# Optimization experiments

Measured on AMD Instinct MI355X. Metric: run time of the kernel, lower is better.

The kernel has to match this reference:

```python
import jax, jax.numpy as jnp
import numpy as np
from math import factorial

LMAX = 4
L2 = (LMAX + 1) ** 2                      # 25 spherical components
RES_B = 2 * (2 * LMAX + 1)                # 18 Gauss-Legendre beta nodes (exact for band 2*lmax products)
RES_A = 2 * (2 * LMAX + 1) + 1            # 19 uniform alpha nodes
EPS = 1e-5
# degree index of each (l,m) slot: [0,1,1,1,2,...]
L_IDX = np.repeat(np.arange(LMAX + 1), 2 * np.arange(LMAX + 1) + 1)


def _assoc_legendre(lmax, x):
    # Associated Legendre P_l^m(x) with Condon-Shortley phase; returns [l, m, B]
    B = x.shape[0]
    P = np.zeros((lmax + 1, lmax + 1, B))
    P[0, 0] = 1.0
    sx = np.sqrt(np.maximum(0.0, 1.0 - x * x))
    for m in range(1, lmax + 1):
        P[m, m] = -(2 * m - 1) * sx * P[m - 1, m - 1]
    for m in range(lmax):
        P[m + 1, m] = (2 * m + 1) * x * P[m, m]
    for m in range(lmax + 1):
        for l in range(m + 2, lmax + 1):
            P[l, m] = ((2 * l - 1) * x * P[l - 1, m] - (l + m - 1) * P[l - 2, m]) / (l - m)
    return P


def _build_sh(lmax, res_b, res_a):
    # Real orthonormal spherical harmonics sampled on a Gauss-Legendre x uniform-phi grid.
    ct, wb = np.polynomial.legendre.leggauss(res_b)       # cos(theta) nodes / weights
    phi = np.arange(res_a) * (2.0 * np.pi / res_a)
    P = _assoc_legendre(lmax, ct)
    l2 = (lmax + 1) ** 2
    Y = np.zeros((res_b, res_a, l2))
    for l in range(lmax + 1):
        for m in range(l + 1):
            Nlm = np.sqrt((2 * l + 1) / (4.0 * np.pi) * factorial(l - m) / factorial(l + m))
            if m == 0:
                Y[:, :, l * l + l] = (Nlm * P[l, 0])[:, None]
            else:
                base = np.sqrt(2.0) * Nlm * P[l, m]
                Y[:, :, l * l + l + m] = base[:, None] * np.cos(m * phi)[None, :]
                Y[:, :, l * l + l - m] = base[:, None] * np.sin(m * phi)[None, :]
    w = (wb[:, None] * np.full((1, res_a), 2.0 * np.pi / res_a)).reshape(-1)
    Yf = Y.reshape(-1, l2)
    return Yf, w

_Y_np, _w_np = _build_sh(LMAX, RES_B, RES_A)
TO_GRID = jnp.asarray(_Y_np, dtype=jnp.float32)                     # [G, L2]
FROM_GRID = jnp.asarray((_w_np[:, None] * _Y_np).T, dtype=jnp.float32)  # [L2, G], exact SH projection


def setup_inputs() -> dict:
    key = jax.random.key(0)
    ks = jax.random.split(key, 8)
    N, C = 6000, 128
    x = jax.random.normal(ks[0], (N, L2, C), dtype=jnp.float32)
    batch = jax.random.randint(ks[1], (N,), 0, 77)
    s = 1.0 / np.sqrt(C)
    return {
        "x": x,
        "batch": batch,
        "norm_w": jnp.ones((LMAX + 1, C), dtype=jnp.float32),
        "norm_b": jnp.zeros((C,), dtype=jnp.float32),
        "w1": jax.random.normal(ks[2], (LMAX + 1, C, C), dtype=jnp.float32) * s,
        "b1": jax.random.normal(ks[3], (C,), dtype=jnp.float32) * 0.02,
        "w_tp": jax.random.normal(ks[4], (LMAX + 1, C), dtype=jnp.float32),
        "w2": jax.random.normal(ks[5], (LMAX + 1, C, C), dtype=jnp.float32) * s,
        "b2": jax.random.normal(ks[6], (C,), dtype=jnp.float32) * 0.02,
    }


def _merge_layer_norm(x, w, b):
    # x: [N, L2, C]; center l=0 over channels, RMS over all components+channels, per-(l,C) affine.
    mean0 = jnp.mean(x[:, 0:1, :], axis=-1, keepdims=True)
    xc = jnp.concatenate([x[:, 0:1, :] - mean0, x[:, 1:, :]], axis=1)
    var = jnp.mean(xc * xc, axis=(1, 2), keepdims=True)
    xn = xc * jax.lax.rsqrt(var + EPS)
    out = xn * w[L_IDX][None]                      # [N, L2, C]
    return jnp.concatenate([out[:, 0:1, :] + b, out[:, 1:, :]], axis=1)


def _so3_linear(x, w, b):
    # per-degree linear: w [lmax+1, out, in]; bias on l=0 only
    W = w[L_IDX]                                    # [L2, out, in]
    y = jnp.einsum('nlc,lkc->nlk', x, W)
    return jnp.concatenate([y[:, 0:1, :] + b, y[:, 1:, :]], axis=1)


def _gaunt_self_tp(x, w_tp):
    # Gaunt self tensor-product (depthwise): pointwise square on the sphere,
    # exact projection back to SH (Gaunt-coefficient contraction), per-(l,C) weight.
    g = jnp.einsum('nlc,gl->ngc', x, TO_GRID)       # [N, G, C] to-grid
    y = jnp.einsum('ngc,lg->nlc', g * g, FROM_GRID)  # [N, L2, C] from-grid
    return y * w_tp[L_IDX][None]


def reference(x, batch, norm_w, norm_b, w1, b1, w_tp, w2, b2):
    x_res = x
    h = _merge_layer_norm(x, norm_w, norm_b)
    h = _so3_linear(h, w1, b1)
    h = _gaunt_self_tp(h, w_tp)
    h = _so3_linear(h, w2, b2)
    return h + x_res  # ffn_shortcut is Identity (num_in == num_out)
```

## Files before the change

kernel.cpp:

```cpp
#include <hip/hip_runtime.h>
#include <math.h>

#define L2C 25
#define CH  128
#define NB  8
#define GLB 7
#define GLA 13
#define NG  91
#define GPAD 96
#define KPAD 32
#define HROWS 242

typedef short bf16x8 __attribute__((ext_vector_type(8)));
typedef short short4v __attribute__((ext_vector_type(4)));
typedef int   i32x4  __attribute__((ext_vector_type(4)));
typedef float f32x4  __attribute__((ext_vector_type(4)));
typedef unsigned uint2v __attribute__((ext_vector_type(2)));

union frag_u { i32x4 i; bf16x8 h; };

__device__ inline short f2bf(float f) {
  union { float f; unsigned u; } v; v.f = f;
  unsigned r = (v.u + 0x7FFFu + ((v.u >> 16) & 1u)) >> 16;
  return (short)r;
}
__device__ inline float bf2f(short s) {
  union { unsigned u; float f; } v; v.u = ((unsigned)(unsigned short)s) << 16; return v.f;
}
__device__ inline unsigned cvt_pk_bf16(float lo, float hi) {
  unsigned r; asm("v_cvt_pk_bf16_f32 %0, %1, %2" : "=v"(r) : "v"(lo), "v"(hi)); return r;
}

__global__ void build_tables_kernel(short* __restrict__ toT, short* __restrict__ frT) {
  const int g = threadIdx.x;
  if (g >= GPAD) return;
  const double PI = 3.14159265358979323846;
  double Y[L2C];
  double wg = 0.0;
  if (g < NG) {
    const int b = g / GLA;
    const int a = g % GLA;
    double xx = cos(PI * (b + 0.75) / (GLB + 0.5));
    double pp = 1.0;
    for (int it = 0; it < 64; ++it) {
      double p0 = 1.0, p1 = xx;
      for (int j = 2; j <= GLB; ++j) { double p2 = ((2.0*j-1.0)*xx*p1 - (j-1.0)*p0)/j; p0 = p1; p1 = p2; }
      pp = GLB * (xx*p1 - p0) / (xx*xx - 1.0);
      xx -= p1 / pp;
    }
    { double p0 = 1.0, p1 = xx;
      for (int j = 2; j <= GLB; ++j) { double p2 = ((2.0*j-1.0)*xx*p1 - (j-1.0)*p0)/j; p0 = p1; p1 = p2; }
      pp = GLB * (xx*p1 - p0) / (xx*xx - 1.0); }
    const double wb = 2.0 / ((1.0 - xx*xx) * pp * pp);
    const double ct = xx;
    const double sx = sqrt(fmax(0.0, 1.0 - ct*ct));
    double P[5][5];
    P[0][0] = 1.0;
    for (int m = 1; m <= 4; ++m) P[m][m] = -(2.0*m - 1.0) * sx * P[m-1][m-1];
    for (int m = 0; m <= 3; ++m) P[m+1][m] = (2.0*m + 1.0) * ct * P[m][m];
    for (int m = 0; m <= 4; ++m)
      for (int l = m + 2; l <= 4; ++l)
        P[l][m] = ((2.0*l-1.0)*ct*P[l-1][m] - (l+m-1.0)*P[l-2][m]) / (l - m);
    const double fact[9] = {1,1,2,6,24,120,720,5040,40320};
    const double phi = (2.0*PI/GLA) * a;
    for (int l = 0; l <= 4; ++l)
      for (int m = 0; m <= l; ++m) {
        double Nlm = sqrt((2.0*l+1.0)/(4.0*PI) * fact[l-m]/fact[l+m]);
        if (m == 0) Y[l*l + l] = Nlm * P[l][0];
        else {
          double base = sqrt(2.0) * Nlm * P[l][m];
          Y[l*l + l + m] = base * cos((double)m * phi);
          Y[l*l + l - m] = base * sin((double)m * phi);
        }
      }
    wg = wb * (2.0*PI/GLA);
  }
  for (int l = 0; l < KPAD; ++l) {
    float tv = (g < NG && l < L2C) ? (float)Y[l] : 0.f;
    toT[g*KPAD + l] = f2bf(tv);
  }
  {
    const int hi = g >> 4, r = g & 15;
    const int ksv = hi >> 1, pa = hi & 1;
    const int lqv = r >> 2,  pb = r & 3;
    const int u  = pa*4 + pb;
    const int kg = ksv*32 + lqv*8 + u;
    for (int l = 0; l < KPAD; ++l)
      frT[l*GPAD + kg] = (g < NG && l < L2C) ? f2bf((float)(wg * Y[l])) : (short)0;
  }
}

__global__ void convert_w_kernel(const float* __restrict__ w1, const float* __restrict__ w2,
                                 short* __restrict__ wb1, short* __restrict__ wb2) {
  const int i = blockIdx.x * 256 + threadIdx.x;
  if (i < 5*CH*CH) { wb1[i] = f2bf(w1[i]); wb2[i] = f2bf(w2[i]); }
}

__global__ __launch_bounds__(512, 2) void eqv3_fused8(
    const float* __restrict__ x,
    const float* __restrict__ norm_w, const float* __restrict__ norm_b,
    const short* __restrict__ wb1, const float* __restrict__ b1,
    const float* __restrict__ w_tp,
    const short* __restrict__ wb2, const float* __restrict__ b2,
    const short* __restrict__ toT, const short* __restrict__ frT,
    float* __restrict__ out)
{
  __shared__ __align__(16) short hsh[16][HROWS][8];
  __shared__ __align__(16) short hg[NB][4][CH][8];

  const int tid  = threadIdx.x;
  const int w    = tid >> 6;
  const int lane = tid & 63;
  const int l16  = lane & 15;
  const int lq   = lane >> 4;
  const long n0  = (long)blockIdx.x * NB;
  const int k    = w*16 + l16;

  constexpr int LDEG[L2C] = {0,1,1,1,2,2,2,2,2,3,3,3,3,3,3,3,4,4,4,4,4,4,4,4,4};
  constexpr int BROW[5]   = {0,16,48,96,160};
  constexpr int NT[5]     = {1,2,3,4,5};

  {
    const i32x4 z = {0,0,0,0};
    #pragma unroll
    for (int n = 0; n < NB; ++n) *(i32x4*)&hg[n][3][k][0] = z;
  }

  {
    const float4* x4 = (const float4*)(x + (n0 + w)*(long)(L2C*CH));
    float4 xv[13];
    float s0 = 0.f, s0q = 0.f, sq = 0.f;
    #pragma unroll
    for (int it = 0; it < 13; ++it) {
      const int j = it*64 + lane;
      if (j < 800) {
        xv[it] = x4[j];
        const float t = xv[it].x*xv[it].x + xv[it].y*xv[it].y + xv[it].z*xv[it].z + xv[it].w*xv[it].w;
        if (j < 32) { s0 += xv[it].x + xv[it].y + xv[it].z + xv[it].w; s0q += t; }
        else        sq += t;
      }
    }
    #pragma unroll
    for (int o = 1; o < 64; o <<= 1) {
      s0  += __shfl_xor(s0,  o, 64);
      s0q += __shfl_xor(s0q, o, 64);
      sq  += __shfl_xor(sq,  o, 64);
    }
    const float mean0 = s0 * (1.f/CH);
    const float var   = (sq + s0q - CH*mean0*mean0) * (1.f/(L2C*CH));
    const float rstd  = rsqrtf(var + 1e-5f);
    #pragma unroll
    for (int it = 0; it < 13; ++it) {
      const int j = it*64 + lane;
      if (j < 800) {
        const int s = j >> 5;
        const int d = (int)sqrtf((float)s + 0.5f);
        const int row = 8*(s + d) + w;
        const int c32 = j & 31;
        const int c0  = c32 * 4;
        const float4 nw4 = ((const float4*)norm_w)[d*32 + c32];
        float a0 = xv[it].x, a1 = xv[it].y, a2 = xv[it].z, a3 = xv[it].w;
        if (s == 0) {
          const float4 nb4 = ((const float4*)norm_b)[c32];
          a0 = (a0 - mean0)*rstd*nw4.x + nb4.x;
          a1 = (a1 - mean0)*rstd*nw4.y + nb4.y;
          a2 = (a2 - mean0)*rstd*nw4.z + nb4.z;
          a3 = (a3 - mean0)*rstd*nw4.w + nb4.w;
        } else {
          a0 *= rstd*nw4.x; a1 *= rstd*nw4.y; a2 *= rstd*nw4.z; a3 *= rstd*nw4.w;
        }
        uint2v pk; pk[0] = cvt_pk_bf16(a0, a1); pk[1] = cvt_pk_bf16(a2, a3);
        *(uint2v*)&hsh[c0 >> 3][row][c0 & 7] = pk;
      }
    }
  }
  __syncthreads();

  {
    const float b1k = b1[k];
    #pragma unroll
    for (int d = 0; d < 5; ++d) {
      frag_u B[4];
      #pragma unroll
      for (int ks = 0; ks < 4; ++ks)
        B[ks].i = *(const i32x4*)(wb1 + ((d*CH + k)*CH + ks*32 + lq*8));
      #pragma unroll
      for (int mt = 0; mt < NT[d]; ++mt) {
        f32x4 acc = {0.f, 0.f, 0.f, 0.f};
        #pragma unroll
        for (int ks = 0; ks < 4; ++ks) {
          const bf16x8 a = *(const bf16x8*)&hsh[ks*4 + lq][BROW[d] + mt*16 + l16][0];
          acc = __builtin_amdgcn_mfma_f32_16x16x32_bf16(a, B[ks].h, acc, 0, 0, 0);
        }
        const int sl = 2*mt + (lq >> 1);
        if (sl <= 2*d) {
          const int s = d*d + sl;
          #pragma unroll
          for (int i = 0; i < 4; ++i)
            hg[(lq & 1)*4 + i][s >> 3][k][s & 7] = f2bf(acc[i] + ((s == 0) ? b1k : 0.f));
        }
      }
    }
  }
  __syncthreads();

  {
    frag_u Ato[6];
    #pragma unroll
    for (int gt = 0; gt < 6; ++gt)
      Ato[gt].i = *(const i32x4*)(toT + (gt*16 + l16)*KPAD + lq*8);
    frag_u Afr[2][3];
    #pragma unroll
    for (int mt = 0; mt < 2; ++mt)
      #pragma unroll
      for (int ks = 0; ks < 3; ++ks)
        Afr[mt][ks].i = *(const i32x4*)(frT + (mt*16 + l16)*GPAD + ks*32 + lq*8);

    frag_u Bh[NB];
    #pragma unroll
    for (int n = 0; n < NB; ++n)
      Bh[n].i = *(const i32x4*)&hg[n][lq][k][0];

    float wtp[2][4]; int hrowb[2][4];
    #pragma unroll
    for (int mt = 0; mt < 2; ++mt)
      #pragma unroll
      for (int i = 0; i < 4; ++i) {
        const int l = mt*16 + lq*4 + i;
        if (l < L2C) {
          const int d = LDEG[l];
          wtp[mt][i]   = w_tp[d*CH + k];
          hrowb[mt][i] = BROW[d] + (l - d*d)*NB;
        } else { wtp[mt][i] = 0.f; hrowb[mt][i] = -1; }
      }

    #pragma unroll
    for (int np = 0; np < 4; ++np) {
      const int nA = np, nB2 = np + 4;
      unsigned pA[6][2], pB[6][2];
      #pragma unroll
      for (int gt = 0; gt < 6; ++gt) {
        f32x4 aA = {0.f,0.f,0.f,0.f}, aB = {0.f,0.f,0.f,0.f};
        aA = __builtin_amdgcn_mfma_f32_16x16x32_bf16(Ato[gt].h, Bh[nA].h,  aA, 0, 0, 0);
        aB = __builtin_amdgcn_mfma_f32_16x16x32_bf16(Ato[gt].h, Bh[nB2].h, aB, 0, 0, 0);
        pA[gt][0] = cvt_pk_bf16(aA[0]*aA[0], aA[1]*aA[1]);
        pA[gt][1] = cvt_pk_bf16(aA[2]*aA[2], aA[3]*aA[3]);
        pB[gt][0] = cvt_pk_bf16(aB[0]*aB[0], aB[1]*aB[1]);
        pB[gt][1] = cvt_pk_bf16(aB[2]*aB[2], aB[3]*aB[3]);
      }
      f32x4 acc2A[2] = {{0.f,0.f,0.f,0.f},{0.f,0.f,0.f,0.f}};
      f32x4 acc2B[2] = {{0.f,0.f,0.f,0.f},{0.f,0.f,0.f,0.f}};
      #pragma unroll
      for (int ks = 0; ks < 3; ++ks) {
        frag_u BgA, BgB;
        BgA.i[0] = (int)pA[2*ks][0];   BgA.i[1] = (int)pA[2*ks][1];
        BgA.i[2] = (int)pA[2*ks+1][0]; BgA.i[3] = (int)pA[2*ks+1][1];
        BgB.i[0] = (int)pB[2*ks][0];   BgB.i[1] = (int)pB[2*ks][1];
        BgB.i[2] = (int)pB[2*ks+1][0]; BgB.i[3] = (int)pB[2*ks+1][1];
        acc2A[0] = __builtin_amdgcn_mfma_f32_16x16x32_bf16(Afr[0][ks].h, BgA.h, acc2A[0], 0, 0, 0);
        acc2A[1] = __builtin_amdgcn_mfma_f32_16x16x32_bf16(Afr[1][ks].h, BgA.h, acc2A[1], 0, 0, 0);
        acc2B[0] = __builtin_amdgcn_mfma_f32_16x16x32_bf16(Afr[0][ks].h, BgB.h, acc2B[0], 0, 0, 0);
        acc2B[1] = __builtin_amdgcn_mfma_f32_16x16x32_bf16(Afr[1][ks].h, BgB.h, acc2B[1], 0, 0, 0);
      }
      #pragma unroll
      for (int mt = 0; mt < 2; ++mt)
        #pragma unroll
        for (int i = 0; i < 4; ++i)
          if (hrowb[mt][i] >= 0) {
            hsh[k >> 3][hrowb[mt][i] + nA][k & 7]  = f2bf(acc2A[mt][i] * wtp[mt][i]);
            hsh[k >> 3][hrowb[mt][i] + nB2][k & 7] = f2bf(acc2B[mt][i] * wtp[mt][i]);
          }
    }
  }
  __syncthreads();

  {
    short* stg = &hg[0][0][0][0];
    const float b2k = b2[k];
    #pragma unroll
    for (int d = 0; d < 5; ++d) {
      frag_u B[4];
      #pragma unroll
      for (int ks = 0; ks < 4; ++ks)
        B[ks].i = *(const i32x4*)(wb2 + ((d*CH + k)*CH + ks*32 + lq*8));
      #pragma unroll
      for (int mt = 0; mt < NT[d]; ++mt) {
        f32x4 acc = {0.f, 0.f, 0.f, 0.f};
        #pragma unroll
        for (int ks = 0; ks < 4; ++ks) {
          const bf16x8 a = *(const bf16x8*)&hsh[ks*4 + lq][BROW[d] + mt*16 + l16][0];
          acc = __builtin_amdgcn_mfma_f32_16x16x32_bf16(a, B[ks].h, acc, 0, 0, 0);
        }
        const int sl = 2*mt + (lq >> 1);
        if (sl <= 2*d) {
          const int s = d*d + sl;
          #pragma unroll
          for (int i = 0; i < 4; ++i) {
            const int node = (lq & 1)*4 + i;
            stg[(node*L2C + s)*CH + k] = f2bf(acc[i] + ((s == 0) ? b2k : 0.f));
          }
        }
      }
    }
  }
  __syncthreads();

  {
    const short* stg = &hg[0][0][0][0];
    const float4* xs = (const float4*)(x + n0*(long)(L2C*CH));
    float4* os = (float4*)(out + n0*(long)(L2C*CH));
    for (int j = tid; j < NB*L2C*CH/4; j += 512) {
      const float4 xv4 = xs[j];
      const short4v sv = *(const short4v*)&stg[j*4];
      float4 o;
      o.x = bf2f(sv[0]) + xv4.x;
      o.y = bf2f(sv[1]) + xv4.y;
      o.z = bf2f(sv[2]) + xv4.z;
      o.w = bf2f(sv[3]) + xv4.w;
      os[j] = o;
    }
  }
}

extern "C" void kernel_launch(void* const* d_in, const int* in_sizes, int n_in,
                              void* d_out, int out_size, void* d_ws, size_t ws_size,
                              hipStream_t stream) {
  const float* x      = (const float*)d_in[0];
  const float* norm_w = (const float*)d_in[2];
  const float* norm_b = (const float*)d_in[3];
  const float* w1     = (const float*)d_in[4];
  const float* b1     = (const float*)d_in[5];
  const float* w_tp   = (const float*)d_in[6];
  const float* w2     = (const float*)d_in[7];
  const float* b2     = (const float*)d_in[8];
  float* out = (float*)d_out;

  const int N = in_sizes[0] / (L2C*CH);

  short* wsS = (short*)d_ws;
  short* toT = wsS;
  short* frT = toT + GPAD*KPAD;
  short* wb1 = frT + KPAD*GPAD;
  short* wb2 = wb1 + 5*CH*CH;

  build_tables_kernel<<<1, 128, 0, stream>>>(toT, frT);
  convert_w_kernel<<<(5*CH*CH + 255)/256, 256, 0, stream>>>(w1, w2, wb1, wb2);
  eqv3_fused8<<<N/NB, 512, 0, stream>>>(x, norm_w, norm_b, wb1, b1, w_tp, wb2, b2, toT, frT, out);
}
```

Measured before the change: 117.7 us.

## Process three node groups per block with register prefetch of next inputs

Each block now loops over three groups of eight nodes, loading the next group's input rows into registers while the current group's tensor-product and second linear run. The residual add reuses the register-held input instead of reloading it from global memory, and per-channel constants are hoisted out of the loop. This reduces the block count to a third, which lowers available parallelism and raises register pressure from the doubled input buffers.

```diff
diff --git a/kernel.cpp b/kernel.cpp
--- a/kernel.cpp
+++ b/kernel.cpp
@@ -4,6 +4,7 @@
 #define L2C 25
 #define CH  128
 #define NB  8
+#define NGRP 3
 #define GLB 7
 #define GLA 13
 #define NG  91
@@ -113,7 +114,6 @@
   const int lane = tid & 63;
   const int l16  = lane & 15;
   const int lq   = lane >> 4;
-  const long n0  = (long)blockIdx.x * NB;
   const int k    = w*16 + l16;
 
   constexpr int LDEG[L2C] = {0,1,1,1,2,2,2,2,2,3,3,3,3,3,3,3,4,4,4,4,4,4,4,4,4};
@@ -126,199 +126,226 @@
     for (int n = 0; n < NB; ++n) *(i32x4*)&hg[n][3][k][0] = z;
   }
 
+  const float b1k = b1[k];
+  const float b2k = b2[k];
+  float wtp[2][4]; int hrowb[2][4];
+  #pragma unroll
+  for (int mt = 0; mt < 2; ++mt)
+    #pragma unroll
+    for (int i = 0; i < 4; ++i) {
+      const int l = mt*16 + lq*4 + i;
+      if (l < L2C) {
+        const int d = LDEG[l];
+        wtp[mt][i]   = w_tp[d*CH + k];
+        hrowb[mt][i] = BROW[d] + (l - d*d)*NB;
+      } else { wtp[mt][i] = 0.f; hrowb[mt][i] = -1; }
+    }
+
+  float4 xv[13], xn[13];
   {
+    const long n0 = (long)blockIdx.x * NGRP * NB;
     const float4* x4 = (const float4*)(x + (n0 + w)*(long)(L2C*CH));
-    float4 xv[13];
-    float s0 = 0.f, s0q = 0.f, sq = 0.f;
     #pragma unroll
     for (int it = 0; it < 13; ++it) {
       const int j = it*64 + lane;
-      if (j < 800) {
-        xv[it] = x4[j];
-        const float t = xv[it].x*xv[it].x + xv[it].y*xv[it].y + xv[it].z*xv[it].z + xv[it].w*xv[it].w;
-        if (j < 32) { s0 += xv[it].x + xv[it].y + xv[it].z + xv[it].w; s0q += t; }
-        else        sq += t;
-      }
-    }
-    #pragma unroll
-    for (int o = 1; o < 64; o <<= 1) {
-      s0  += __shfl_xor(s0,  o, 64);
-      s0q += __shfl_xor(s0q, o, 64);
-      sq  += __shfl_xor(sq,  o, 64);
-    }
-    const float mean0 = s0 * (1.f/CH);
-    const float var   = (sq + s0q - CH*mean0*mean0) * (1.f/(L2C*CH));
-    const float rstd  = rsqrtf(var + 1e-5f);
-    #pragma unroll
-    for (int it = 0; it < 13; ++it) {
-      const int j = it*64 + lane;
-      if (j < 800) {
-        const int s = j >> 5;
-        const int d = (int)sqrtf((float)s + 0.5f);
-        const int row = 8*(s + d) + w;
-        const int c32 = j & 31;
-        const int c0  = c32 * 4;
-        const float4 nw4 = ((const float4*)norm_w)[d*32 + c32];
-        float a0 = xv[it].x, a1 = xv[it].y, a2 = xv[it].z, a3 = xv[it].w;
-        if (s == 0) {
-          const float4 nb4 = ((const float4*)norm_b)[c32];
-          a0 = (a0 - mean0)*rstd*nw4.x + nb4.x;
-          a1 = (a1 - mean0)*rstd*nw4.y + nb4.y;
-          a2 = (a2 - mean0)*rstd*nw4.z + nb4.z;
-          a3 = (a3 - mean0)*rstd*nw4.w + nb4.w;
-        } else {
-          a0 *= rstd*nw4.x; a1 *= rstd*nw4.y; a2 *= rstd*nw4.z; a3 *= rstd*nw4.w;
-        }
-        uint2v pk; pk[0] = cvt_pk_bf16(a0, a1); pk[1] = cvt_pk_bf16(a2, a3);
-        *(uint2v*)&hsh[c0 >> 3][row][c0 & 7] = pk;
-      }
-    }
-  }
-  __syncthreads();
-
-  {
-    const float b1k = b1[k];
-    #pragma unroll
-    for (int d = 0; d < 5; ++d) {
-      frag_u B[4];
-      #pragma unroll
-      for (int ks = 0; ks < 4; ++ks)
-        B[ks].i = *(const i32x4*)(wb1 + ((d*CH + k)*CH + ks*32 + lq*8));
-      #pragma unroll
-      for (int mt = 0; mt < NT[d]; ++mt) {
-        f32x4 acc = {0.f, 0.f, 0.f, 0.f};
-        #pragma unroll
-        for (int ks = 0; ks < 4; ++ks) {
-          const bf16x8 a = *(const bf16x8*)&hsh[ks*4 + lq][BROW[d] + mt*16 + l16][0];
-          acc = __builtin_amdgcn_mfma_f32_16x16x32_bf16(a, B[ks].h, acc, 0, 0, 0);
-        }
-        const int sl = 2*mt + (lq >> 1);
-        if (sl <= 2*d) {
-          const int s = d*d + sl;
+      if (j < 800) xv[it] = x4[j];
+    }
+  }
+
+  for (int grp = 0; grp < NGRP; ++grp) {
+    const long n0 = ((long)blockIdx.x * NGRP + grp) * NB;
+
+    {
+      float s0 = 0.f, s0q = 0.f, sq = 0.f;
+      #pragma unroll
+      for (int it = 0; it < 13; ++it) {
+        const int j = it*64 + lane;
+        if (j < 800) {
+          const float t = xv[it].x*xv[it].x + xv[it].y*xv[it].y + xv[it].z*xv[it].z + xv[it].w*xv[it].w;
+          if (j < 32) { s0 += xv[it].x + xv[it].y + xv[it].z + xv[it].w; s0q += t; }
+          else        sq += t;
+        }
+      }
+      #pragma unroll
+      for (int o = 1; o < 64; o <<= 1) {
+        s0  += __shfl_xor(s0,  o, 64);
+        s0q += __shfl_xor(s0q, o, 64);
+        sq  += __shfl_xor(sq,  o, 64);
+      }
+      const float mean0 = s0 * (1.f/CH);
+      const float var   = (sq + s0q - CH*mean0*mean0) * (1.f/(L2C*CH));
+      const float rstd  = rsqrtf(var + 1e-5f);
+      #pragma unroll
+      for (int it = 0; it < 13; ++it) {
+        const int j = it*64 + lane;
+        if (j < 800) {
+          const int s = j >> 5;
+          const int d = (int)sqrtf((float)s + 0.5f);
+          const int row = 8*(s + d) + w;
+          const int c32 = j & 31;
+          const int c0  = c32 * 4;
+          const float4 nw4 = ((const float4*)norm_w)[d*32 + c32];
+          float a0 = xv[it].x, a1 = xv[it].y, a2 = xv[it].z, a3 = xv[it].w;
+          if (s == 0) {
+            const float4 nb4 = ((const float4*)norm_b)[c32];
+            a0 = (a0 - mean0)*rstd*nw4.x + nb4.x;
+            a1 = (a1 - mean0)*rstd*nw4.y + nb4.y;
+            a2 = (a2 - mean0)*rstd*nw4.z + nb4.z;
+            a3 = (a3 - mean0)*rstd*nw4.w + nb4.w;
+          } else {
+            a0 *= rstd*nw4.x; a1 *= rstd*nw4.y; a2 *= rstd*nw4.z; a3 *= rstd*nw4.w;
+          }
+          uint2v pk; pk[0] = cvt_pk_bf16(a0, a1); pk[1] = cvt_pk_bf16(a2, a3);
+          *(uint2v*)&hsh[c0 >> 3][row][c0 & 7] = pk;
+        }
+      }
+    }
+    __syncthreads();
+
+    {
+      #pragma unroll
+      for (int d = 0; d < 5; ++d) {
+        frag_u B[4];
+        #pragma unroll
+        for (int ks = 0; ks < 4; ++ks)
+          B[ks].i = *(const i32x4*)(wb1 + ((d*CH + k)*CH + ks*32 + lq*8));
+        #pragma unroll
+        for (int mt = 0; mt < NT[d]; ++mt) {
+          f32x4 acc = {0.f, 0.f, 0.f, 0.f};
           #pragma unroll
-          for (int i = 0; i < 4; ++i)
-            hg[(lq & 1)*4 + i][s >> 3][k][s & 7] = f2bf(acc[i] + ((s == 0) ? b1k : 0.f));
-        }
-      }
-    }
-  }
-  __syncthreads();
-
-  {
-    frag_u Ato[6];
-    #pragma unroll
-    for (int gt = 0; gt < 6; ++gt)
-      Ato[gt].i = *(const i32x4*)(toT + (gt*16 + l16)*KPAD + lq*8);
-    frag_u Afr[2][3];
-    #pragma unroll
-    for (int mt = 0; mt < 2; ++mt)
-      #pragma unroll
-      for (int ks = 0; ks < 3; ++ks)
-        Afr[mt][ks].i = *(const i32x4*)(frT + (mt*16 + l16)*GPAD + ks*32 + lq*8);
-
+          for (int ks = 0; ks < 4; ++ks) {
+            const bf16x8 a = *(const bf16x8*)&hsh[ks*4 + lq][BROW[d] + mt*16 + l16][0];
+            acc = __builtin_amdgcn_mfma_f32_16x16x32_bf16(a, B[ks].h, acc, 0, 0, 0);
+          }
+          const int sl = 2*mt + (lq >> 1);
+          if (sl <= 2*d) {
+            const int s = d*d + sl;
+            #pragma unroll
+            for (int i = 0; i < 4; ++i)
+              hg[(lq & 1)*4 + i][s >> 3][k][s & 7] = f2bf(acc[i] + ((s == 0) ? b1k : 0.f));
+          }
+        }
+      }
+    }
     frag_u Bh[NB];
     #pragma unroll
     for (int n = 0; n < NB; ++n)
       Bh[n].i = *(const i32x4*)&hg[n][lq][k][0];
-
-    float wtp[2][4]; int hrowb[2][4];
-    #pragma unroll
-    for (int mt = 0; mt < 2; ++mt)
-      #pragma unroll
-      for (int i = 0; i < 4; ++i) {
-        const int l = mt*16 + lq*4 + i;
-        if (l < L2C) {
-          const int d = LDEG[l];
-          wtp[mt][i]   = w_tp[d*CH + k];
-          hrowb[mt][i] = BROW[d] + (l - d*d)*NB;
-        } else { wtp[mt][i] = 0.f; hrowb[mt][i] = -1; }
-      }
-
-    #pragma unroll
-    for (int np = 0; np < 4; ++np) {
-      const int nA = np, nB2 = np + 4;
-      unsigned pA[6][2], pB[6][2];
-      #pragma unroll
-      for (int gt = 0; gt < 6; ++gt) {
-        f32x4 aA = {0.f,0.f,0.f,0.f}, aB = {0.f,0.f,0.f,0.f};
-        aA = __builtin_amdgcn_mfma_f32_16x16x32_bf16(Ato[gt].h, Bh[nA].h,  aA, 0, 0, 0);
-        aB = __builtin_amdgcn_mfma_f32_16x16x32_bf16(Ato[gt].h, Bh[nB2].h, aB, 0, 0, 0);
-        pA[gt][0] = cvt_pk_bf16(aA[0]*aA[0], aA[1]*aA[1]);
-        pA[gt][1] = cvt_pk_bf16(aA[2]*aA[2], aA[3]*aA[3]);
-        pB[gt][0] = cvt_pk_bf16(aB[0]*aB[0], aB[1]*aB[1]);
-        pB[gt][1] = cvt_pk_bf16(aB[2]*aB[2], aB[3]*aB[3]);
-      }
-      f32x4 acc2A[2] = {{0.f,0.f,0.f,0.f},{0.f,0.f,0.f,0.f}};
-      f32x4 acc2B[2] = {{0.f,0.f,0.f,0.f},{0.f,0.f,0.f,0.f}};
-      #pragma unroll
-      for (int ks = 0; ks < 3; ++ks) {
-        frag_u BgA, BgB;
-        BgA.i[0] = (int)pA[2*ks][0];   BgA.i[1] = (int)pA[2*ks][1];
-        BgA.i[2] = (int)pA[2*ks+1][0]; BgA.i[3] = (int)pA[2*ks+1][1];
-        BgB.i[0] = (int)pB[2*ks][0];   BgB.i[1] = (int)pB[2*ks][1];
-        BgB.i[2] = (int)pB[2*ks+1][0]; BgB.i[3] = (int)pB[2*ks+1][1];
-        acc2A[0] = __builtin_amdgcn_mfma_f32_16x16x32_bf16(Afr[0][ks].h, BgA.h, acc2A[0], 0, 0, 0);
-        acc2A[1] = __builtin_amdgcn_mfma_f32_16x16x32_bf16(Afr[1][ks].h, BgA.h, acc2A[1], 0, 0, 0);
-        acc2B[0] = __builtin_amdgcn_mfma_f32_16x16x32_bf16(Afr[0][ks].h, BgB.h, acc2B[0], 0, 0, 0);
-        acc2B[1] = __builtin_amdgcn_mfma_f32_16x16x32_bf16(Afr[1][ks].h, BgB.h, acc2B[1], 0, 0, 0);
-      }
+    __syncthreads();
+
+    {
+      frag_u Ato[6];
+      #pragma unroll
+      for (int gt = 0; gt < 6; ++gt)
+        Ato[gt].i = *(const i32x4*)(toT + (gt*16 + l16)*KPAD + lq*8);
+      frag_u Afr[2][3];
       #pragma unroll
       for (int mt = 0; mt < 2; ++mt)
         #pragma unroll
-        for (int i = 0; i < 4; ++i)
-          if (hrowb[mt][i] >= 0) {
-            hsh[k >> 3][hrowb[mt][i] + nA][k & 7]  = f2bf(acc2A[mt][i] * wtp[mt][i]);
-            hsh[k >> 3][hrowb[mt][i] + nB2][k & 7] = f2bf(acc2B[mt][i] * wtp[mt][i]);
-          }
-    }
-  }
-  __syncthreads();
-
-  {
-    short* stg = &hg[0][0][0][0];
-    const float b2k = b2[k];
-    #pragma unroll
-    for (int d = 0; d < 5; ++d) {
-      frag_u B[4];
-      #pragma unroll
-      for (int ks = 0; ks < 4; ++ks)
-        B[ks].i = *(const i32x4*)(wb2 + ((d*CH + k)*CH + ks*32 + lq*8));
-      #pragma unroll
-      for (int mt = 0; mt < NT[d]; ++mt) {
-        f32x4 acc = {0.f, 0.f, 0.f, 0.f};
-        #pragma unroll
-        for (int ks = 0; ks < 4; ++ks) {
-          const bf16x8 a = *(const bf16x8*)&hsh[ks*4 + lq][BROW[d] + mt*16 + l16][0];
-          acc = __builtin_amdgcn_mfma_f32_16x16x32_bf16(a, B[ks].h, acc, 0, 0, 0);
-        }
-        const int sl = 2*mt + (lq >> 1);
-        if (sl <= 2*d) {
-          const int s = d*d + sl;
+        for (int ks = 0; ks < 3; ++ks)
+          Afr[mt][ks].i = *(const i32x4*)(frT + (mt*16 + l16)*GPAD + ks*32 + lq*8);
+
+      #pragma unroll
+      for (int np = 0; np < 4; ++np) {
+        const int nA = np, nB2 = np + 4;
+        unsigned pA[6][2], pB[6][2];
+        #pragma unroll
+        for (int gt = 0; gt < 6; ++gt) {
+          f32x4 aA = {0.f,0.f,0.f,0.f}, aB = {0.f,0.f,0.f,0.f};
+          aA = __builtin_amdgcn_mfma_f32_16x16x32_bf16(Ato[gt].h, Bh[nA].h,  aA, 0, 0, 0);
+          aB = __builtin_amdgcn_mfma_f32_16x16x32_bf16(Ato[gt].h, Bh[nB2].h, aB, 0, 0, 0);
+          pA[gt][0] = cvt_pk_bf16(aA[0]*aA[0], aA[1]*aA[1]);
+          pA[gt][1] = cvt_pk_bf16(aA[2]*aA[2], aA[3]*aA[3]);
+          pB[gt][0] = cvt_pk_bf16(aB[0]*aB[0], aB[1]*aB[1]);
+          pB[gt][1] = cvt_pk_bf16(aB[2]*aB[2], aB[3]*aB[3]);
+        }
+        f32x4 acc2A[2] = {{0.f,0.f,0.f,0.f},{0.f,0.f,0.f,0.f}};
+        f32x4 acc2B[2] = {{0.f,0.f,0.f,0.f},{0.f,0.f,0.f,0.f}};
+        #pragma unroll
+        for (int ks = 0; ks < 3; ++ks) {
+          frag_u BgA, BgB;
+          BgA.i[0] = (int)pA[2*ks][0];   BgA.i[1] = (int)pA[2*ks][1];
+          BgA.i[2] = (int)pA[2*ks+1][0]; BgA.i[3] = (int)pA[2*ks+1][1];
+          BgB.i[0] = (int)pB[2*ks][0];   BgB.i[1] = (int)pB[2*ks][1];
+          BgB.i[2] = (int)pB[2*ks+1][0]; BgB.i[3] = (int)pB[2*ks+1][1];
+          acc2A[0] = __builtin_amdgcn_mfma_f32_16x16x32_bf16(Afr[0][ks].h, BgA.h, acc2A[0], 0, 0, 0);
+          acc2A[1] = __builtin_amdgcn_mfma_f32_16x16x32_bf16(Afr[1][ks].h, BgA.h, acc2A[1], 0, 0, 0);
+          acc2B[0] = __builtin_amdgcn_mfma_f32_16x16x32_bf16(Afr[0][ks].h, BgB.h, acc2B[0], 0, 0, 0);
+          acc2B[1] = __builtin_amdgcn_mfma_f32_16x16x32_bf16(Afr[1][ks].h, BgB.h, acc2B[1], 0, 0, 0);
+        }
+        #pragma unroll
+        for (int mt = 0; mt < 2; ++mt)
           #pragma unroll
-          for (int i = 0; i < 4; ++i) {
-            const int node = (lq & 1)*4 + i;
-            stg[(node*L2C + s)*CH + k] = f2bf(acc[i] + ((s == 0) ? b2k : 0.f));
-          }
-        }
-      }
-    }
-  }
-  __syncthreads();
-
-  {
-    const short* stg = &hg[0][0][0][0];
-    const float4* xs = (const float4*)(x + n0*(long)(L2C*CH));
-    float4* os = (float4*)(out + n0*(long)(L2C*CH));
-    for (int j = tid; j < NB*L2C*CH/4; j += 512) {
-      const float4 xv4 = xs[j];
-      const short4v sv = *(const short4v*)&stg[j*4];
-      float4 o;
-      o.x = bf2f(sv[0]) + xv4.x;
-      o.y = bf2f(sv[1]) + xv4.y;
-      o.z = bf2f(sv[2]) + xv4.z;
-      o.w = bf2f(sv[3]) + xv4.w;
-      os[j] = o;
-    }
+          for (int i = 0; i < 4; ++i)
+            if (hrowb[mt][i] >= 0) {
+              hsh[k >> 3][hrowb[mt][i] + nA][k & 7]  = f2bf(acc2A[mt][i] * wtp[mt][i]);
+              hsh[k >> 3][hrowb[mt][i] + nB2][k & 7] = f2bf(acc2B[mt][i] * wtp[mt][i]);
+            }
+      }
+    }
+
+    if (grp < NGRP - 1) {
+      const float4* x4n = (const float4*)(x + (n0 + NB + w)*(long)(L2C*CH));
+      #pragma unroll
+      for (int it = 0; it < 13; ++it) {
+        const int j = it*64 + lane;
+        if (j < 800) xn[it] = x4n[j];
+      }
+    }
+    __syncthreads();
+
+    {
+      short* stg = &hg[0][0][0][0];
+      #pragma unroll
+      for (int d = 0; d < 5; ++d) {
+        frag_u B[4];
+        #pragma unroll
+        for (int ks = 0; ks < 4; ++ks)
+          B[ks].i = *(const i32x4*)(wb2 + ((d*CH + k)*CH + ks*32 + lq*8));
+        #pragma unroll
+        for (int mt = 0; mt < NT[d]; ++mt) {
+          f32x4 acc = {0.f, 0.f, 0.f, 0.f};
+          #pragma unroll
+          for (int ks = 0; ks < 4; ++ks) {
+            const bf16x8 a = *(const bf16x8*)&hsh[ks*4 + lq][BROW[d] + mt*16 + l16][0];
+            acc = __builtin_amdgcn_mfma_f32_16x16x32_bf16(a, B[ks].h, acc, 0, 0, 0);
+          }
+          const int sl = 2*mt + (lq >> 1);
+          if (sl <= 2*d) {
+            const int s = d*d + sl;
+            #pragma unroll
+            for (int i = 0; i < 4; ++i) {
+              const int node = (lq & 1)*4 + i;
+              stg[(node*L2C + s)*CH + k] = f2bf(acc[i] + ((s == 0) ? b2k : 0.f));
+            }
+          }
+        }
+      }
+    }
+    __syncthreads();
+
+    {
+      const short* stg = &hg[0][0][0][0];
+      float4* os = (float4*)(out + (n0 + w)*(long)(L2C*CH));
+      #pragma unroll
+      for (int it = 0; it < 13; ++it) {
+        const int j = it*64 + lane;
+        if (j < 800) {
+          const short4v sv = *(const short4v*)&stg[w*(L2C*CH) + j*4];
+          float4 o;
+          o.x = bf2f(sv[0]) + xv[it].x;
+          o.y = bf2f(sv[1]) + xv[it].y;
+          o.z = bf2f(sv[2]) + xv[it].z;
+          o.w = bf2f(sv[3]) + xv[it].w;
+          os[j] = o;
+        }
+      }
+    }
+    if (grp < NGRP - 1) {
+      #pragma unroll
+      for (int it = 0; it < 13; ++it) xv[it] = xn[it];
+    }
+    __syncthreads();
   }
 }
 
@@ -336,6 +363,7 @@
   float* out = (float*)d_out;
 
   const int N = in_sizes[0] / (L2C*CH);
+  const int nblk = N / (NB * NGRP);
 
   short* wsS = (short*)d_ws;
   short* toT = wsS;
@@ -345,5 +373,5 @@
 
   build_tables_kernel<<<1, 128, 0, stream>>>(toT, frT);
   convert_w_kernel<<<(5*CH*CH + 255)/256, 256, 0, stream>>>(w1, w2, wb1, wb2);
-  eqv3_fused8<<<N/NB, 512, 0, stream>>>(x, norm_w, norm_b, wb1, b1, w_tp, wb2, b2, toT, frT, out);
-}
+  eqv3_fused8<<<nblk, 512, 0, stream>>>(x, norm_w, norm_b, wb1, b1, w_tp, wb2, b2, toT, frT, out);
+}
```

Result: slower. 205.1 us (+74.2%).

## Alias LDS buffers into one union and write output directly from MFMA results

Applied to the files above, without the earlier changes.

Both shared-memory arrays now share a single 64 KB buffer. Linear-1 results are held in registers as packed bf16 and written to the grid buffer only after a barrier, and the grid-input fragments are loaded before the next barrier. Launch bounds rise to 4 blocks per CU to allow higher occupancy. The final staging pass is removed: linear-2 writes fp32 output plus the residual straight to global memory, which drops one bf16 rounding but replaces coalesced float4 stores with strided scalar loads and stores, and puts more pressure on registers.

```diff
diff --git a/kernel.cpp b/kernel.cpp
--- a/kernel.cpp
+++ b/kernel.cpp
@@ -12,7 +12,6 @@
 #define HROWS 242
 
 typedef short bf16x8 __attribute__((ext_vector_type(8)));
-typedef short short4v __attribute__((ext_vector_type(4)));
 typedef int   i32x4  __attribute__((ext_vector_type(4)));
 typedef float f32x4  __attribute__((ext_vector_type(4)));
 typedef unsigned uint2v __attribute__((ext_vector_type(2)));
@@ -23,9 +22,6 @@
   union { float f; unsigned u; } v; v.f = f;
   unsigned r = (v.u + 0x7FFFu + ((v.u >> 16) & 1u)) >> 16;
   return (short)r;
-}
-__device__ inline float bf2f(short s) {
-  union { unsigned u; float f; } v; v.u = ((unsigned)(unsigned short)s) << 16; return v.f;
 }
 __device__ inline unsigned cvt_pk_bf16(float lo, float hi) {
   unsigned r; asm("v_cvt_pk_bf16_f32 %0, %1, %2" : "=v"(r) : "v"(lo), "v"(hi)); return r;
@@ -83,8 +79,7 @@
     const int hi = g >> 4, r = g & 15;
     const int ksv = hi >> 1, pa = hi & 1;
     const int lqv = r >> 2,  pb = r & 3;
-    const int u  = pa*4 + pb;
-    const int kg = ksv*32 + lqv*8 + u;
+    const int kg = ksv*32 + lqv*8 + pa*4 + pb;
     for (int l = 0; l < KPAD; ++l)
       frT[l*GPAD + kg] = (g < NG && l < L2C) ? f2bf((float)(wg * Y[l])) : (short)0;
   }
@@ -96,7 +91,7 @@
   if (i < 5*CH*CH) { wb1[i] = f2bf(w1[i]); wb2[i] = f2bf(w2[i]); }
 }
 
-__global__ __launch_bounds__(512, 2) void eqv3_fused8(
+__global__ __launch_bounds__(512, 4) void eqv3_fused8u(
     const float* __restrict__ x,
     const float* __restrict__ norm_w, const float* __restrict__ norm_b,
     const short* __restrict__ wb1, const float* __restrict__ b1,
@@ -105,8 +100,9 @@
     const short* __restrict__ toT, const short* __restrict__ frT,
     float* __restrict__ out)
 {
-  __shared__ __align__(16) short hsh[16][HROWS][8];
-  __shared__ __align__(16) short hg[NB][4][CH][8];
+  __shared__ __align__(16) short u[32768];
+  short (*hsh)[HROWS][8] = (short (*)[HROWS][8])u;
+  short (*hg)[4][CH][8]  = (short (*)[4][CH][8])u;
 
   const int tid  = threadIdx.x;
   const int w    = tid >> 6;
@@ -119,12 +115,6 @@
   constexpr int LDEG[L2C] = {0,1,1,1,2,2,2,2,2,3,3,3,3,3,3,3,4,4,4,4,4,4,4,4,4};
   constexpr int BROW[5]   = {0,16,48,96,160};
   constexpr int NT[5]     = {1,2,3,4,5};
-
-  {
-    const i32x4 z = {0,0,0,0};
-    #pragma unroll
-    for (int n = 0; n < NB; ++n) *(i32x4*)&hg[n][3][k][0] = z;
-  }
 
   {
     const float4* x4 = (const float4*)(x + (n0 + w)*(long)(L2C*CH));
@@ -176,8 +166,10 @@
   }
   __syncthreads();
 
+  unsigned pk1[15][2];
   {
     const float b1k = b1[k];
+    int t = 0;
     #pragma unroll
     for (int d = 0; d < 5; ++d) {
       frag_u B[4];
@@ -185,7 +177,7 @@
       for (int ks = 0; ks < 4; ++ks)
         B[ks].i = *(const i32x4*)(wb1 + ((d*CH + k)*CH + ks*32 + lq*8));
       #pragma unroll
-      for (int mt = 0; mt < NT[d]; ++mt) {
+      for (int mt = 0; mt < NT[d]; ++mt, ++t) {
         f32x4 acc = {0.f, 0.f, 0.f, 0.f};
         #pragma unroll
         for (int ks = 0; ks < 4; ++ks) {
@@ -193,15 +185,39 @@
           acc = __builtin_amdgcn_mfma_f32_16x16x32_bf16(a, B[ks].h, acc, 0, 0, 0);
         }
         const int sl = 2*mt + (lq >> 1);
+        const float bb = ((d == 0) & (sl == 0)) ? b1k : 0.f;
+        pk1[t][0] = cvt_pk_bf16(acc[0] + bb, acc[1] + bb);
+        pk1[t][1] = cvt_pk_bf16(acc[2] + bb, acc[3] + bb);
+      }
+    }
+  }
+  __syncthreads();
+
+  {
+    const i32x4 z = {0,0,0,0};
+    #pragma unroll
+    for (int n = 0; n < NB; ++n) *(i32x4*)&hg[n][3][k][0] = z;
+    int t = 0;
+    #pragma unroll
+    for (int d = 0; d < 5; ++d)
+      #pragma unroll
+      for (int mt = 0; mt < NT[d]; ++mt, ++t) {
+        const int sl = 2*mt + (lq >> 1);
         if (sl <= 2*d) {
-          const int s = d*d + sl;
-          #pragma unroll
-          for (int i = 0; i < 4; ++i)
-            hg[(lq & 1)*4 + i][s >> 3][k][s & 7] = f2bf(acc[i] + ((s == 0) ? b1k : 0.f));
-        }
-      }
-    }
-  }
+          const int s  = d*d + sl;
+          const int nb = (lq & 1)*4;
+          hg[nb+0][s >> 3][k][s & 7] = (short)(pk1[t][0] & 0xFFFFu);
+          hg[nb+1][s >> 3][k][s & 7] = (short)(pk1[t][0] >> 16);
+          hg[nb+2][s >> 3][k][s & 7] = (short)(pk1[t][1] & 0xFFFFu);
+          hg[nb+3][s >> 3][k][s & 7] = (short)(pk1[t][1] >> 16);
+        }
+      }
+  }
+
+  frag_u Bh[NB];
+  #pragma unroll
+  for (int n = 0; n < NB; ++n)
+    Bh[n].i = *(const i32x4*)&hg[n][lq][k][0];
   __syncthreads();
 
   {
@@ -215,11 +231,6 @@
       #pragma unroll
       for (int ks = 0; ks < 3; ++ks)
         Afr[mt][ks].i = *(const i32x4*)(frT + (mt*16 + l16)*GPAD + ks*32 + lq*8);
-
-    frag_u Bh[NB];
-    #pragma unroll
-    for (int n = 0; n < NB; ++n)
-      Bh[n].i = *(const i32x4*)&hg[n][lq][k][0];
 
     float wtp[2][4]; int hrowb[2][4];
     #pragma unroll
@@ -275,7 +286,6 @@
   __syncthreads();
 
   {
-    short* stg = &hg[0][0][0][0];
     const float b2k = b2[k];
     #pragma unroll
     for (int d = 0; d < 5; ++d) {
@@ -297,27 +307,11 @@
           #pragma unroll
           for (int i = 0; i < 4; ++i) {
             const int node = (lq & 1)*4 + i;
-            stg[(node*L2C + s)*CH + k] = f2bf(acc[i] + ((s == 0) ? b2k : 0.f));
+            const long base = (n0 + node)*(long)(L2C*CH) + s*CH + k;
+            out[base] = acc[i] + ((s == 0) ? b2k : 0.f) + x[base];
           }
         }
       }
-    }
-  }
-  __syncthreads();
-
-  {
-    const short* stg = &hg[0][0][0][0];
-    const float4* xs = (const float4*)(x + n0*(long)(L2C*CH));
-    float4* os = (float4*)(out + n0*(long)(L2C*CH));
-    for (int j = tid; j < NB*L2C*CH/4; j += 512) {
-      const float4 xv4 = xs[j];
-      const short4v sv = *(const short4v*)&stg[j*4];
-      float4 o;
-      o.x = bf2f(sv[0]) + xv4.x;
-      o.y = bf2f(sv[1]) + xv4.y;
-      o.z = bf2f(sv[2]) + xv4.z;
-      o.w = bf2f(sv[3]) + xv4.w;
-      os[j] = o;
     }
   }
 }
@@ -345,5 +339,5 @@
 
   build_tables_kernel<<<1, 128, 0, stream>>>(toT, frT);
   convert_w_kernel<<<(5*CH*CH + 255)/256, 256, 0, stream>>>(w1, w2, wb1, wb2);
-  eqv3_fused8<<<N/NB, 512, 0, stream>>>(x, norm_w, norm_b, wb1, b1, w_tp, wb2, b2, toT, frT, out);
-}
+  eqv3_fused8u<<<N/NB, 512, 0, stream>>>(x, norm_w, norm_b, wb1, b1, w_tp, wb2, b2, toT, frT, out);
+}
```

Measured after the change: 114.1 us. 1.03x faster.
